# Kernel tuning notes

Hardware: AMD Instinct MI355X
Metric: run time of the kernel (lower is better)

Reference implementation:

```python
import jax, jax.numpy as jnp
import numpy as np

D_MODEL = 512
NHEAD = 8
D_K = D_MODEL // NHEAD
SCALE = float(np.sqrt(D_K))


def setup_inputs() -> dict:
    key = jax.random.key(0)
    ks = jax.random.split(key, 11)
    B, S = 2, 4096
    std = 1.0 / np.sqrt(D_MODEL)
    inp = {
        'q': jax.random.normal(ks[0], (B, S, D_MODEL), jnp.float32),
        'k': jax.random.normal(ks[1], (B, S, D_MODEL), jnp.float32),
        'v': jax.random.normal(ks[2], (B, S, D_MODEL), jnp.float32),
        'w_q': jax.random.normal(ks[3], (D_MODEL, D_MODEL), jnp.float32) * std,
        'b_q': jax.random.normal(ks[4], (D_MODEL,), jnp.float32) * std,
        'w_k': jax.random.normal(ks[5], (D_MODEL, D_MODEL), jnp.float32) * std,
        'b_k': jax.random.normal(ks[6], (D_MODEL,), jnp.float32) * std,
        'w_v': jax.random.normal(ks[7], (D_MODEL, D_MODEL), jnp.float32) * std,
        'b_v': jax.random.normal(ks[8], (D_MODEL,), jnp.float32) * std,
        'w_o': jax.random.normal(ks[9], (D_MODEL, D_MODEL), jnp.float32) * std,
        'b_o': jax.random.normal(ks[10], (D_MODEL,), jnp.float32) * std,
    }
    return inp


def reference(q, k, v, w_q, b_q, w_k, b_k, w_v, b_v, w_o, b_o):
    B, S, _ = q.shape
    # torch Linear: y = x @ W.T + b
    def proj(x, W, b):
        y = x @ W.T + b
        return y.reshape(B, -1, NHEAD, D_K).transpose(0, 2, 1, 3)  # [B,H,S,Dk]
    qh = proj(q, w_q, b_q)
    kh = proj(k, w_k, b_k)
    vh = proj(v, w_v, b_v)
    scores = jnp.einsum('bhsd,bhtd->bhst', qh, kh) / SCALE  # [B,H,S,S]
    attn = jax.nn.softmax(scores, axis=-1)
    out = jnp.einsum('bhst,bhtd->bhsd', attn, vh)  # [B,H,S,Dk]
    out = out.transpose(0, 2, 1, 3).reshape(B, S, D_MODEL)
    return out @ w_o.T + b_o
```

## Files before the change

### kernel.cpp

```cpp
#include <hip/hip_runtime.h>
#include <stdint.h>

#define DM 512
#define S_LEN 4096
#define NH 8
#define DK 64

typedef __attribute__((ext_vector_type(8))) short bf16x8;
typedef __attribute__((ext_vector_type(4))) float f32x4;

#define QSCALE 0.18033688011112042f
#define NEGBIAS -17.312340490667562f

__device__ inline ushort f2bf(float f) {
  union { float f; uint32_t u; } v; v.f = f;
  uint32_t r = v.u + 0x7fff + ((v.u >> 16) & 1);
  return (ushort)(r >> 16);
}
__device__ inline uint32_t fu(float f) {
  union { float f; uint32_t u; } v; v.f = f; return v.u;
}
__device__ inline uint32_t pktrunc(float lo, float hi) {
  return __builtin_amdgcn_perm(fu(hi), fu(lo), 0x07060302);
}

__device__ inline void async_cp16(const void* g, void* l) {
  __builtin_amdgcn_global_load_lds((const __attribute__((address_space(1))) void*)g,
                                   (__attribute__((address_space(3))) void*)l, 16, 0, 0);
}

__global__ __launch_bounds__(256) void cvt_all(
    const float4* __restrict__ s0, ushort* __restrict__ d0,
    const float4* __restrict__ s1, ushort* __restrict__ d1,
    const float4* __restrict__ s2, ushort* __restrict__ d2,
    const float4* __restrict__ s3, ushort* __restrict__ d3,
    const float4* __restrict__ x0, ushort* __restrict__ y0,
    const float4* __restrict__ x1, ushort* __restrict__ y1,
    const float4* __restrict__ x2, ushort* __restrict__ y2) {
  if (blockIdx.x < 256) {
    int i = blockIdx.x * 256 + threadIdx.x;
    { float4 v = s0[i]; ushort4 o = {f2bf(v.x), f2bf(v.y), f2bf(v.z), f2bf(v.w)}; *(ushort4*)&d0[i * 4] = o; }
    { float4 v = s1[i]; ushort4 o = {f2bf(v.x), f2bf(v.y), f2bf(v.z), f2bf(v.w)}; *(ushort4*)&d1[i * 4] = o; }
    { float4 v = s2[i]; ushort4 o = {f2bf(v.x), f2bf(v.y), f2bf(v.z), f2bf(v.w)}; *(ushort4*)&d2[i * 4] = o; }
    { float4 v = s3[i]; ushort4 o = {f2bf(v.x), f2bf(v.y), f2bf(v.z), f2bf(v.w)}; *(ushort4*)&d3[i * 4] = o; }
  } else {
    int b = blockIdx.x - 256;
    #pragma unroll
    for (int r = 0; r < 2; r++) {
      int i = (b * 2 + r) * 256 + threadIdx.x;
      { float4 v = x0[i]; ushort4 o = {f2bf(v.x), f2bf(v.y), f2bf(v.z), f2bf(v.w)}; *(ushort4*)&y0[i * 4] = o; }
      { float4 v = x1[i]; ushort4 o = {f2bf(v.x), f2bf(v.y), f2bf(v.z), f2bf(v.w)}; *(ushort4*)&y1[i * 4] = o; }
      { float4 v = x2[i]; ushort4 o = {f2bf(v.x), f2bf(v.y), f2bf(v.z), f2bf(v.w)}; *(ushort4*)&y2[i * 4] = o; }
    }
  }
}

__global__ __launch_bounds__(256) void gemm_proj(
    const ushort* __restrict__ xq, const ushort* __restrict__ xk, const ushort* __restrict__ xv,
    const ushort* __restrict__ wq, const ushort* __restrict__ wk, const ushort* __restrict__ wv,
    const float* __restrict__ bq, const float* __restrict__ bk, const float* __restrict__ bv,
    ushort* __restrict__ Qh, ushort* __restrict__ Kh, ushort* __restrict__ VhT) {
  const ushort* A; const ushort* Bt; const float* bias; float cs;
  if (blockIdx.z == 0)      { A = xq; Bt = wq; bias = bq; cs = QSCALE; }
  else if (blockIdx.z == 1) { A = xk; Bt = wk; bias = bk; cs = 1.0f; }
  else                      { A = xv; Bt = wv; bias = bv; cs = 1.0f; }

  __shared__ ushort Asp[3][2048];
  __shared__ ushort Bsp[3][4096];
  const int tid = threadIdx.x;
  const int w = tid >> 6, lane = tid & 63;
  const int quad = lane >> 4, l16 = lane & 15;
  const int wm = w >> 1, wn = w & 1;
  const int m0 = blockIdx.x * 64, n0 = blockIdx.y * 128;
  const f32x4 zero4 = {0.f, 0.f, 0.f, 0.f};

  f32x4 acc[2][4];
  #pragma unroll
  for (int i = 0; i < 2; i++)
    #pragma unroll
    for (int j = 0; j < 4; j++) acc[i][j] = zero4;

  #define PSTAGE(KB, BUF) do {                                                        \
    const int k0_ = (KB) * 32;                                                        \
    ushort* asp_ = &Asp[BUF][0];                                                      \
    ushort* bsp_ = &Bsp[BUF][0];                                                      \
    { int idx = tid;               \
      int row = idx >> 2, c = (idx & 3) ^ ((row >> 1) & 3);                           \
      async_cp16(&A[(size_t)(m0 + row) * DM + k0_ + c * 8], &asp_[idx * 8]); }        \
    _Pragma("unroll")                                                                 \
    for (int r_ = 0; r_ < 2; r_++) {                                \
      int idx = r_ * 256 + tid;                                                       \
      int row = idx >> 2, c = (idx & 3) ^ ((row >> 1) & 3);                           \
      async_cp16(&Bt[(size_t)(n0 + row) * DM + k0_ + c * 8], &bsp_[idx * 8]);         \
    }                                                                                 \
  } while (0)

  PSTAGE(0, 0);
  PSTAGE(1, 1);

  #pragma unroll
  for (int kb = 0; kb < 16; kb++) {
    if (kb < 15) asm volatile("s_waitcnt vmcnt(3)" ::: "memory");
    else         asm volatile("s_waitcnt vmcnt(0)" ::: "memory");
    __builtin_amdgcn_s_barrier();
    __builtin_amdgcn_sched_barrier(0);
    if (kb < 14) PSTAGE(kb + 2, (kb + 2) % 3);
    const int cur = kb % 3;
    bf16x8 af[2], bfr[4];
    #pragma unroll
    for (int i = 0; i < 2; i++) {
      int r = wm * 32 + i * 16 + l16;
      af[i] = *(const bf16x8*)&Asp[cur][r * 32 + ((quad ^ ((r >> 1) & 3)) << 3)];
    }
    #pragma unroll
    for (int j = 0; j < 4; j++) {
      int rb = wn * 64 + j * 16 + l16;
      bfr[j] = *(const bf16x8*)&Bsp[cur][rb * 32 + ((quad ^ ((rb >> 1) & 3)) << 3)];
    }
    #pragma unroll
    for (int i = 0; i < 2; i++)
      #pragma unroll
      for (int j = 0; j < 4; j++)
        acc[i][j] = __builtin_amdgcn_mfma_f32_16x16x32_bf16(af[i], bfr[j], acc[i][j], 0, 0, 0);
  }

  if (blockIdx.z != 2) {
    ushort* C = (blockIdx.z == 0) ? Qh : Kh;
    #pragma unroll
    for (int j = 0; j < 4; j++) {
      int col_g = n0 + wn * 64 + j * 16 + l16;
      float bv = bias[col_g];
      int h = col_g >> 6, d = col_g & 63;
      #pragma unroll
      for (int i = 0; i < 2; i++) {
        #pragma unroll
        for (int r = 0; r < 4; r++) {
          int row_g = m0 + wm * 32 + i * 16 + quad * 4 + r;
          int b = row_g >> 12, s = row_g & 4095;
          C[(((size_t)(b * NH + h) << 12) + s) * DK + d] = f2bf((acc[i][j][r] + bv) * cs);
        }
      }
    }
  } else {
    #pragma unroll
    for (int j = 0; j < 4; j++) {
      int col_g = n0 + wn * 64 + j * 16 + l16;
      float bv = bias[col_g];
      int h = col_g >> 6, d = col_g & 63;
      #pragma unroll
      for (int i = 0; i < 2; i++) {
        int row0 = m0 + wm * 32 + i * 16 + quad * 4;
        int b = row0 >> 12, s0 = row0 & 4095;
        int sl = s0 & 31;
        int sp = (s0 & ~31) | (((sl >> 2) & 3) << 3) | (((sl >> 4) & 1) << 2);
        ushort4 pk = {f2bf(acc[i][j][0] + bv), f2bf(acc[i][j][1] + bv),
                      f2bf(acc[i][j][2] + bv), f2bf(acc[i][j][3] + bv)};
        *(ushort4*)&VhT[((size_t)(b * NH + h) * DK + d) * S_LEN + sp] = pk;
      }
    }
  }
}

__global__ __launch_bounds__(256) void gemm_out(const ushort* __restrict__ A,
                                                const ushort* __restrict__ Bt,
                                                const float* __restrict__ bias,
                                                float* __restrict__ C) {
  __shared__ ushort Asp[3][2048];
  __shared__ ushort Bsp[3][4096];
  const int tid = threadIdx.x;
  const int w = tid >> 6, lane = tid & 63;
  const int quad = lane >> 4, l16 = lane & 15;
  const int wm = w >> 1, wn = w & 1;
  const int m0 = blockIdx.x * 64, n0 = blockIdx.y * 128;
  const f32x4 zero4 = {0.f, 0.f, 0.f, 0.f};

  f32x4 acc[2][4];
  #pragma unroll
  for (int i = 0; i < 2; i++)
    #pragma unroll
    for (int j = 0; j < 4; j++) acc[i][j] = zero4;

  #define OSTAGE(KB, BUF) do {                                                        \
    const int k0_ = (KB) * 32;                                                        \
    ushort* asp_ = &Asp[BUF][0];                                                      \
    ushort* bsp_ = &Bsp[BUF][0];                                                      \
    { int idx = tid;                                                                  \
      int row = idx >> 2, c = (idx & 3) ^ ((row >> 1) & 3);                           \
      async_cp16(&A[(size_t)(m0 + row) * DM + k0_ + c * 8], &asp_[idx * 8]); }        \
    _Pragma("unroll")                                                                 \
    for (int r_ = 0; r_ < 2; r_++) {                                                  \
      int idx = r_ * 256 + tid;                                                       \
      int row = idx >> 2, c = (idx & 3) ^ ((row >> 1) & 3);                           \
      async_cp16(&Bt[(size_t)(n0 + row) * DM + k0_ + c * 8], &bsp_[idx * 8]);         \
    }                                                                                 \
  } while (0)

  OSTAGE(0, 0);
  OSTAGE(1, 1);

  #pragma unroll
  for (int kb = 0; kb < 16; kb++) {
    if (kb < 15) asm volatile("s_waitcnt vmcnt(3)" ::: "memory");
    else         asm volatile("s_waitcnt vmcnt(0)" ::: "memory");
    __builtin_amdgcn_s_barrier();
    __builtin_amdgcn_sched_barrier(0);
    if (kb < 14) OSTAGE(kb + 2, (kb + 2) % 3);
    const int cur = kb % 3;
    bf16x8 af[2], bfr[4];
    #pragma unroll
    for (int i = 0; i < 2; i++) {
      int r = wm * 32 + i * 16 + l16;
      af[i] = *(const bf16x8*)&Asp[cur][r * 32 + ((quad ^ ((r >> 1) & 3)) << 3)];
    }
    #pragma unroll
    for (int j = 0; j < 4; j++) {
      int rb = wn * 64 + j * 16 + l16;
      bfr[j] = *(const bf16x8*)&Bsp[cur][rb * 32 + ((quad ^ ((rb >> 1) & 3)) << 3)];
    }
    #pragma unroll
    for (int i = 0; i < 2; i++)
      #pragma unroll
      for (int j = 0; j < 4; j++)
        acc[i][j] = __builtin_amdgcn_mfma_f32_16x16x32_bf16(af[i], bfr[j], acc[i][j], 0, 0, 0);
  }

  #pragma unroll
  for (int j = 0; j < 4; j++) {
    int col_g = n0 + wn * 64 + j * 16 + l16;
    float bv = bias[col_g];
    #pragma unroll
    for (int i = 0; i < 2; i++) {
      #pragma unroll
      for (int r = 0; r < 4; r++) {
        int row_g = m0 + wm * 32 + i * 16 + quad * 4 + r;
        C[(size_t)row_g * DM + col_g] = acc[i][j][r] + bv;
      }
    }
  }
}

typedef union { bf16x8 v; uint32_t u[4]; } pfu;

__global__ __launch_bounds__(512, 4) void attn(const ushort* __restrict__ Qh,
                                               const ushort* __restrict__ Kh,
                                               const ushort* __restrict__ VhT,
                                               ushort* __restrict__ O) {
  __shared__ ushort smem[2][16384];
  const int tid = threadIdx.x;
  const int w = tid >> 6, lane = tid & 63;
  const int quad = lane >> 4, l16 = lane & 15;
  const int half = w >> 2;
  const int qw = w & 3;
  const int bh = blockIdx.x;
  const int q0 = blockIdx.y * 128 + qw * 32;
  const size_t base = (size_t)bh * S_LEN * DK;
  const f32x4 zero4 = {0.f, 0.f, 0.f, 0.f};
  const f32x4 negb = {NEGBIAS, NEGBIAS, NEGBIAS, NEGBIAS};
  const short one_bf = (short)0x3F80;
  const bf16x8 ones = {one_bf, one_bf, one_bf, one_bf, one_bf, one_bf, one_bf, one_bf};

  if (blockIdx.y >= 16) {
    #pragma unroll
    for (int i = 0; i < 6; i++) __builtin_amdgcn_s_sleep(7);
  }

  bf16x8 qf[2][2];
  #pragma unroll
  for (int i = 0; i < 2; i++)
    #pragma unroll
    for (int c = 0; c < 2; c++)
      qf[i][c] = *(const bf16x8*)&Qh[base + (size_t)(q0 + i * 16 + l16) * DK + c * 32 + quad * 8];

  f32x4 o[2][4];
  f32x4 l_acc[2];
  #pragma unroll
  for (int i = 0; i < 2; i++) {
    l_acc[i] = zero4;
    #pragma unroll
    for (int n = 0; n < 4; n++) o[i][n] = zero4;
  }

  #define STAGE(IT, BUF) do {                                                         \
    const int t0_ = (IT) * 128;                                                       \
    _Pragma("unroll")                                                                 \
    for (int r_ = 0; r_ < 2; r_++) {                                                  \
      int idx = r_ * 512 + tid;                                                       \
      int row = idx >> 3;                                                             \
      int cl = ((idx & 7) << 4) ^ ((row & 7) << 4);                                   \
      async_cp16(&Kh[base + (size_t)(t0_ + row) * DK + (cl >> 1)], &smem[BUF][idx * 8]); \
    }                                                                                 \
    _Pragma("unroll")                                                                 \
    for (int r_ = 0; r_ < 2; r_++) {                                                  \
      int idx = r_ * 512 + tid;                                                       \
      int row = idx >> 4;                                                             \
      int cl = ((idx & 15) << 4) ^ ((row & 7) << 4);                                  \
      async_cp16(&VhT[base + (size_t)row * S_LEN + t0_ + (cl >> 1)], &smem[BUF][8192 + idx * 8]); \
    }                                                                                 \
  } while (0)

  STAGE(0, 0);
  __syncthreads();

  const int swz = (l16 & 7) << 4;

  for (int it = 0; it < 32; it++) {
    const int cur = it & 1;
    if (it < 31) STAGE(it + 1, cur ^ 1);
    const ushort* Kb = &smem[cur][0];
    const ushort* Vb = &smem[cur][8192];

    bf16x8 kf[4][2];
    #pragma unroll
    for (int s = 0; s < 4; s++) {
      int row = half * 64 + s * 16 + l16;
      kf[s][0] = *(const bf16x8*)&Kb[row * 64 + ((( 0 + quad * 16) ^ swz) >> 1)];
      kf[s][1] = *(const bf16x8*)&Kb[row * 64 + (((64 + quad * 16) ^ swz) >> 1)];
    }
    f32x4 sc[2][4];
    __builtin_amdgcn_s_setprio(1);
    #pragma unroll
    for (int i = 0; i < 2; i++)
      #pragma unroll
      for (int s = 0; s < 4; s++) {
        f32x4 t = negb;
        t = __builtin_amdgcn_mfma_f32_16x16x32_bf16(kf[s][0], qf[i][0], t, 0, 0, 0);
        t = __builtin_amdgcn_mfma_f32_16x16x32_bf16(kf[s][1], qf[i][1], t, 0, 0, 0);
        sc[i][s] = t;
      }
    __builtin_amdgcn_s_setprio(0);
    float p[2][4][4];
    #pragma unroll
    for (int i = 0; i < 2; i++)
      #pragma unroll
      for (int s = 0; s < 4; s++)
        #pragma unroll
        for (int r = 0; r < 4; r++)
          p[i][s][r] = __builtin_amdgcn_exp2f(sc[i][s][r]);
    pfu pf[2][2];
    #pragma unroll
    for (int i = 0; i < 2; i++)
      #pragma unroll
      for (int ppl = 0; ppl < 2; ppl++) {
        int s0 = ppl * 2, s1 = ppl * 2 + 1;
        pf[i][ppl].u[0] = pktrunc(p[i][s0][0], p[i][s0][1]);
        pf[i][ppl].u[1] = pktrunc(p[i][s0][2], p[i][s0][3]);
        pf[i][ppl].u[2] = pktrunc(p[i][s1][0], p[i][s1][1]);
        pf[i][ppl].u[3] = pktrunc(p[i][s1][2], p[i][s1][3]);
        l_acc[i] = __builtin_amdgcn_mfma_f32_16x16x32_bf16(pf[i][ppl].v, ones, l_acc[i], 0, 0, 0);
      }
    bf16x8 vf[4][2];
    #pragma unroll
    for (int n = 0; n < 4; n++) {
      int row = n * 16 + l16;
      #pragma unroll
      for (int ppl = 0; ppl < 2; ppl++)
        vf[n][ppl] = *(const bf16x8*)&Vb[row * 128 + ((((half * 2 + ppl) * 64 + quad * 16) ^ swz) >> 1)];
    }
    __builtin_amdgcn_s_setprio(1);
    #pragma unroll
    for (int n = 0; n < 4; n++)
      #pragma unroll
      for (int ppl = 0; ppl < 2; ppl++)
        #pragma unroll
        for (int i = 0; i < 2; i++)
          o[i][n] = __builtin_amdgcn_mfma_f32_16x16x32_bf16(pf[i][ppl].v, vf[n][ppl], o[i][n], 0, 0, 0);
    __builtin_amdgcn_s_setprio(0);

    __syncthreads();
  }

  float* red = (float*)smem;
  const int roff = (qw * 64 + lane) * 40;
  if (half == 1) {
    #pragma unroll
    for (int i = 0; i < 2; i++) {
      #pragma unroll
      for (int n = 0; n < 4; n++)
        *(f32x4*)&red[roff + (i * 4 + n) * 4] = o[i][n];
      *(f32x4*)&red[roff + 32 + i * 4] = l_acc[i];
    }
  }
  __syncthreads();
  if (half == 0) {
    #pragma unroll
    for (int i = 0; i < 2; i++) {
      #pragma unroll
      for (int n = 0; n < 4; n++)
        o[i][n] += *(const f32x4*)&red[roff + (i * 4 + n) * 4];
      l_acc[i] += *(const f32x4*)&red[roff + 32 + i * 4];
    }
    const int b = bh >> 3, h = bh & 7;
    #pragma unroll
    for (int i = 0; i < 2; i++) {
      #pragma unroll
      for (int r = 0; r < 4; r++) {
        float inv = 1.0f / l_acc[i][r];
        int qq = q0 + i * 16 + quad * 4 + r;
        #pragma unroll
        for (int n = 0; n < 4; n++) {
          int d = n * 16 + l16;
          O[(size_t)(b * S_LEN + qq) * DM + h * DK + d] = f2bf(o[i][n][r] * inv);
        }
      }
    }
  }
}

extern "C" void kernel_launch(void* const* d_in, const int* in_sizes, int n_in,
                              void* d_out, int out_size, void* d_ws, size_t ws_size,
                              hipStream_t stream) {
  const float* q   = (const float*)d_in[0];
  const float* k   = (const float*)d_in[1];
  const float* v   = (const float*)d_in[2];
  const float* w_q = (const float*)d_in[3];
  const float* b_q = (const float*)d_in[4];
  const float* w_k = (const float*)d_in[5];
  const float* b_k = (const float*)d_in[6];
  const float* w_v = (const float*)d_in[7];
  const float* b_v = (const float*)d_in[8];
  const float* w_o = (const float*)d_in[9];
  const float* b_o = (const float*)d_in[10];

  const size_t W_ELEMS = (size_t)DM * DM;
  const size_t X_ELEMS = (size_t)2 * S_LEN * DM;
  const size_t HEADS_ELEMS = (size_t)2 * NH * S_LEN * DK;
  ushort* wqb = (ushort*)d_ws;
  ushort* wkb = wqb + W_ELEMS;
  ushort* wvb = wkb + W_ELEMS;
  ushort* wob = wvb + W_ELEMS;
  ushort* Xq  = wob + W_ELEMS;
  ushort* Xk  = Xq + X_ELEMS;
  ushort* Xv  = Xk + X_ELEMS;
  ushort* Qh  = Xv + X_ELEMS;
  ushort* Kh  = Qh + HEADS_ELEMS;
  ushort* VhT = Kh + HEADS_ELEMS;
  ushort* AttO = VhT + HEADS_ELEMS;

  cvt_all<<<2304, 256, 0, stream>>>((const float4*)w_q, wqb, (const float4*)w_k, wkb,
                                    (const float4*)w_v, wvb, (const float4*)w_o, wob,
                                    (const float4*)q, Xq, (const float4*)k, Xk,
                                    (const float4*)v, Xv);
  gemm_proj<<<dim3(128, 4, 3), 256, 0, stream>>>(Xq, Xk, Xv, wqb, wkb, wvb,
                                                 b_q, b_k, b_v, Qh, Kh, VhT);
  attn<<<dim3(16, 32), 512, 0, stream>>>(Qh, Kh, VhT, AttO);
  gemm_out<<<dim3(128, 4), 256, 0, stream>>>(AttO, wob, b_o, (float*)d_out);
}
```

Before: 210.2 us.

## Fuse fp32-to-bf16 activation conversion into projection GEMM A-tile loads

Drops the separate conversion pass over q/k/v. The projection GEMM now loads fp32 activations into registers, truncates them to bf16 and writes them to LDS, while B tiles keep using async global-to-LDS copies. This avoids writing and re-reading 24 MB of bf16 activation copies and one kernel's work, but the GEMM now reads twice the A bytes (with each A tile loaded by 4 column-block CTAs). The pipeline moves to register double-buffering with explicit waitcnt and barriers. Rounding also changes from round-to-nearest to truncation.

```diff
diff --git a/kernel.cpp b/kernel.cpp
--- a/kernel.cpp
+++ b/kernel.cpp
@@ -29,41 +29,26 @@
                                    (__attribute__((address_space(3))) void*)l, 16, 0, 0);
 }
 
-__global__ __launch_bounds__(256) void cvt_all(
-    const float4* __restrict__ s0, ushort* __restrict__ d0,
-    const float4* __restrict__ s1, ushort* __restrict__ d1,
-    const float4* __restrict__ s2, ushort* __restrict__ d2,
-    const float4* __restrict__ s3, ushort* __restrict__ d3,
-    const float4* __restrict__ x0, ushort* __restrict__ y0,
-    const float4* __restrict__ x1, ushort* __restrict__ y1,
-    const float4* __restrict__ x2, ushort* __restrict__ y2) {
-  if (blockIdx.x < 256) {
-    int i = blockIdx.x * 256 + threadIdx.x;
-    { float4 v = s0[i]; ushort4 o = {f2bf(v.x), f2bf(v.y), f2bf(v.z), f2bf(v.w)}; *(ushort4*)&d0[i * 4] = o; }
-    { float4 v = s1[i]; ushort4 o = {f2bf(v.x), f2bf(v.y), f2bf(v.z), f2bf(v.w)}; *(ushort4*)&d1[i * 4] = o; }
-    { float4 v = s2[i]; ushort4 o = {f2bf(v.x), f2bf(v.y), f2bf(v.z), f2bf(v.w)}; *(ushort4*)&d2[i * 4] = o; }
-    { float4 v = s3[i]; ushort4 o = {f2bf(v.x), f2bf(v.y), f2bf(v.z), f2bf(v.w)}; *(ushort4*)&d3[i * 4] = o; }
-  } else {
-    int b = blockIdx.x - 256;
-    #pragma unroll
-    for (int r = 0; r < 2; r++) {
-      int i = (b * 2 + r) * 256 + threadIdx.x;
-      { float4 v = x0[i]; ushort4 o = {f2bf(v.x), f2bf(v.y), f2bf(v.z), f2bf(v.w)}; *(ushort4*)&y0[i * 4] = o; }
-      { float4 v = x1[i]; ushort4 o = {f2bf(v.x), f2bf(v.y), f2bf(v.z), f2bf(v.w)}; *(ushort4*)&y1[i * 4] = o; }
-      { float4 v = x2[i]; ushort4 o = {f2bf(v.x), f2bf(v.y), f2bf(v.z), f2bf(v.w)}; *(ushort4*)&y2[i * 4] = o; }
-    }
-  }
+__global__ __launch_bounds__(256) void cvt_w(const float4* __restrict__ s0, ushort* __restrict__ d0,
+                                             const float4* __restrict__ s1, ushort* __restrict__ d1,
+                                             const float4* __restrict__ s2, ushort* __restrict__ d2,
+                                             const float4* __restrict__ s3, ushort* __restrict__ d3) {
+  int i = blockIdx.x * 256 + threadIdx.x;
+  { float4 v = s0[i]; ushort4 o = {f2bf(v.x), f2bf(v.y), f2bf(v.z), f2bf(v.w)}; *(ushort4*)&d0[i * 4] = o; }
+  { float4 v = s1[i]; ushort4 o = {f2bf(v.x), f2bf(v.y), f2bf(v.z), f2bf(v.w)}; *(ushort4*)&d1[i * 4] = o; }
+  { float4 v = s2[i]; ushort4 o = {f2bf(v.x), f2bf(v.y), f2bf(v.z), f2bf(v.w)}; *(ushort4*)&d2[i * 4] = o; }
+  { float4 v = s3[i]; ushort4 o = {f2bf(v.x), f2bf(v.y), f2bf(v.z), f2bf(v.w)}; *(ushort4*)&d3[i * 4] = o; }
 }
 
 __global__ __launch_bounds__(256) void gemm_proj(
-    const ushort* __restrict__ xq, const ushort* __restrict__ xk, const ushort* __restrict__ xv,
+    const float* __restrict__ q, const float* __restrict__ k, const float* __restrict__ v,
     const ushort* __restrict__ wq, const ushort* __restrict__ wk, const ushort* __restrict__ wv,
     const float* __restrict__ bq, const float* __restrict__ bk, const float* __restrict__ bv,
     ushort* __restrict__ Qh, ushort* __restrict__ Kh, ushort* __restrict__ VhT) {
-  const ushort* A; const ushort* Bt; const float* bias; float cs;
-  if (blockIdx.z == 0)      { A = xq; Bt = wq; bias = bq; cs = QSCALE; }
-  else if (blockIdx.z == 1) { A = xk; Bt = wk; bias = bk; cs = 1.0f; }
-  else                      { A = xv; Bt = wv; bias = bv; cs = 1.0f; }
+  const float* A; const ushort* Bt; const float* bias; float cs;
+  if (blockIdx.z == 0)      { A = q; Bt = wq; bias = bq; cs = QSCALE; }
+  else if (blockIdx.z == 1) { A = k; Bt = wk; bias = bk; cs = 1.0f; }
+  else                      { A = v; Bt = wv; bias = bv; cs = 1.0f; }
 
   __shared__ ushort Asp[3][2048];
   __shared__ ushort Bsp[3][4096];
@@ -80,31 +65,51 @@
     #pragma unroll
     for (int j = 0; j < 4; j++) acc[i][j] = zero4;
 
-  #define PSTAGE(KB, BUF) do {                                                        \
+  const int arow = tid >> 2;
+  const int ac = (tid & 3) ^ ((arow >> 1) & 3);
+  const float* abase = &A[(size_t)(m0 + arow) * DM + ac * 8];
+  float4 ra0, ra1, rb0, rb1;
+
+  #define A_ISSUE(KB, R0, R1) do {                                                    \
+    const float* p_ = abase + (KB) * 32;                                              \
+    R0 = *(const float4*)p_; R1 = *(const float4*)(p_ + 4);                           \
+  } while (0)
+
+  #define A_WRITE(BUF, R0, R1) do {                                                   \
+    uint4 w_ = {pktrunc(R0.x, R0.y), pktrunc(R0.z, R0.w),                             \
+                pktrunc(R1.x, R1.y), pktrunc(R1.z, R1.w)};                            \
+    *(uint4*)&Asp[BUF][tid * 8] = w_;                                                 \
+  } while (0)
+
+  #define PSTAGE_B(KB, BUF) do {                                                      \
     const int k0_ = (KB) * 32;                                                        \
-    ushort* asp_ = &Asp[BUF][0];                                                      \
     ushort* bsp_ = &Bsp[BUF][0];                                                      \
-    { int idx = tid;               \
-      int row = idx >> 2, c = (idx & 3) ^ ((row >> 1) & 3);                           \
-      async_cp16(&A[(size_t)(m0 + row) * DM + k0_ + c * 8], &asp_[idx * 8]); }        \
     _Pragma("unroll")                                                                 \
-    for (int r_ = 0; r_ < 2; r_++) {                                \
+    for (int r_ = 0; r_ < 2; r_++) {                                                  \
       int idx = r_ * 256 + tid;                                                       \
       int row = idx >> 2, c = (idx & 3) ^ ((row >> 1) & 3);                           \
       async_cp16(&Bt[(size_t)(n0 + row) * DM + k0_ + c * 8], &bsp_[idx * 8]);         \
     }                                                                                 \
   } while (0)
 
-  PSTAGE(0, 0);
-  PSTAGE(1, 1);
+  A_ISSUE(0, ra0, ra1);
+  PSTAGE_B(0, 0);
+  asm volatile("" ::: "memory");
+  A_ISSUE(1, rb0, rb1);
+  PSTAGE_B(1, 1);
+  asm volatile("s_waitcnt vmcnt(4)" ::: "memory");
+  A_WRITE(0, ra0, ra1);
+  asm volatile("s_waitcnt lgkmcnt(0)" ::: "memory");
+  __builtin_amdgcn_s_barrier();
+  __builtin_amdgcn_sched_barrier(0);
 
   #pragma unroll
   for (int kb = 0; kb < 16; kb++) {
-    if (kb < 15) asm volatile("s_waitcnt vmcnt(3)" ::: "memory");
-    else         asm volatile("s_waitcnt vmcnt(0)" ::: "memory");
-    __builtin_amdgcn_s_barrier();
-    __builtin_amdgcn_sched_barrier(0);
-    if (kb < 14) PSTAGE(kb + 2, (kb + 2) % 3);
+    if (kb < 14) {
+      if ((kb & 1) == 0) A_ISSUE(kb + 2, ra0, ra1);
+      else               A_ISSUE(kb + 2, rb0, rb1);
+      PSTAGE_B(kb + 2, (kb + 2) % 3);
+    }
     const int cur = kb % 3;
     bf16x8 af[2], bfr[4];
     #pragma unroll
@@ -122,6 +127,15 @@
       #pragma unroll
       for (int j = 0; j < 4; j++)
         acc[i][j] = __builtin_amdgcn_mfma_f32_16x16x32_bf16(af[i], bfr[j], acc[i][j], 0, 0, 0);
+    if (kb < 15) {
+      if (kb < 14) asm volatile("s_waitcnt vmcnt(4)" ::: "memory");
+      else         asm volatile("s_waitcnt vmcnt(0)" ::: "memory");
+      if ((kb & 1) == 0) A_WRITE((kb + 1) % 3, rb0, rb1);
+      else               A_WRITE((kb + 1) % 3, ra0, ra1);
+      asm volatile("s_waitcnt lgkmcnt(0)" ::: "memory");
+      __builtin_amdgcn_s_barrier();
+      __builtin_amdgcn_sched_barrier(0);
+    }
   }
 
   if (blockIdx.z != 2) {
@@ -422,25 +436,19 @@
   const float* b_o = (const float*)d_in[10];
 
   const size_t W_ELEMS = (size_t)DM * DM;
-  const size_t X_ELEMS = (size_t)2 * S_LEN * DM;
   const size_t HEADS_ELEMS = (size_t)2 * NH * S_LEN * DK;
   ushort* wqb = (ushort*)d_ws;
   ushort* wkb = wqb + W_ELEMS;
   ushort* wvb = wkb + W_ELEMS;
   ushort* wob = wvb + W_ELEMS;
-  ushort* Xq  = wob + W_ELEMS;
-  ushort* Xk  = Xq + X_ELEMS;
-  ushort* Xv  = Xk + X_ELEMS;
-  ushort* Qh  = Xv + X_ELEMS;
+  ushort* Qh  = wob + W_ELEMS;
   ushort* Kh  = Qh + HEADS_ELEMS;
   ushort* VhT = Kh + HEADS_ELEMS;
   ushort* AttO = VhT + HEADS_ELEMS;
 
-  cvt_all<<<2304, 256, 0, stream>>>((const float4*)w_q, wqb, (const float4*)w_k, wkb,
-                                    (const float4*)w_v, wvb, (const float4*)w_o, wob,
-                                    (const float4*)q, Xq, (const float4*)k, Xk,
-                                    (const float4*)v, Xv);
-  gemm_proj<<<dim3(128, 4, 3), 256, 0, stream>>>(Xq, Xk, Xv, wqb, wkb, wvb,
+  cvt_w<<<256, 256, 0, stream>>>((const float4*)w_q, wqb, (const float4*)w_k, wkb,
+                                 (const float4*)w_v, wvb, (const float4*)w_o, wob);
+  gemm_proj<<<dim3(128, 4, 3), 256, 0, stream>>>(q, k, v, wqb, wkb, wvb,
                                                  b_q, b_k, b_v, Qh, Kh, VhT);
   attn<<<dim3(16, 32), 512, 0, stream>>>(Qh, Kh, VhT, AttO);
   gemm_out<<<dim3(128, 4), 256, 0, stream>>>(AttO, wob, b_o, (float*)d_out);
```

Measured after the change: 213.6 us. Within noise of the previous version (+1.6%).
